# Performance work log

Hardware: AMD Instinct MI355X
Metric: run time of the kernel (lower is better)

## Reference

```python
import jax, jax.numpy as jnp
import numpy as np

B, S, D = 2, 2048, 2048
H, KVH, HD = 32, 8, 64
GROUPS = H // KVH  # 4
NEG = -1e9


def setup_inputs() -> dict:
    key = jax.random.key(0)
    ks = jax.random.split(key, 5)
    x = jax.random.normal(ks[0], (B, S, D), dtype=jnp.float32)
    # causal additive mask [1,1,S,S]
    causal = jnp.triu(jnp.full((S, S), NEG, dtype=jnp.float32), k=1)[None, None]
    Wq = jax.random.normal(ks[1], (D, D), dtype=jnp.float32) * (D ** -0.5)
    Wk = jax.random.normal(ks[2], (KVH * HD, D), dtype=jnp.float32) * (D ** -0.5)
    Wv = jax.random.normal(ks[3], (KVH * HD, D), dtype=jnp.float32) * (D ** -0.5)
    Wo = jax.random.normal(ks[4], (D, D), dtype=jnp.float32) * (D ** -0.5)
    return {"x": x, "attention_mask": causal, "Wq": Wq, "Wk": Wk, "Wv": Wv, "Wo": Wo}


def reference(x, attention_mask, Wq, Wk, Wv, Wo):
    b, s, _ = x.shape
    # projections (nn.Linear: y = x @ W.T)
    q = (x @ Wq.T).reshape(b, s, H, HD).transpose(0, 2, 1, 3)      # [b,H,s,hd]
    k = (x @ Wk.T).reshape(b, s, KVH, HD).transpose(0, 2, 1, 3)    # [b,KVH,s,hd]
    v = (x @ Wv.T).reshape(b, s, KVH, HD).transpose(0, 2, 1, 3)
    new_kv_cache = (k, v)
    # repeat_interleave over head dim for GQA
    k = jnp.repeat(k, GROUPS, axis=1)  # [b,H,s,hd]
    v = jnp.repeat(v, GROUPS, axis=1)
    scale = 1.0 / jnp.sqrt(jnp.float32(HD))
    scores = jnp.einsum('bhqd,bhkd->bhqk', q, k) * scale
    scores = scores + attention_mask
    attn = jax.nn.softmax(scores.astype(jnp.float32), axis=-1).astype(q.dtype)
    out = jnp.einsum('bhqk,bhkd->bhqd', attn, v)  # [b,H,s,hd]
    out = out.transpose(0, 2, 1, 3).reshape(b, s, H * HD)
    output = out @ Wo.T
    return (output, new_kv_cache[0], new_kv_cache[1])
```

## Files before the change

### kernel.cpp

```cpp
#include <hip/hip_runtime.h>
#include <hip/hip_bf16.h>
#include <stdint.h>

#define B_ 2
#define S_ 2048
#define D_ 2048
#define H_ 32
#define KVH_ 8
#define HD_ 64

typedef __bf16 bf16x8 __attribute__((ext_vector_type(8)));
typedef float f32x4 __attribute__((ext_vector_type(4)));

#define MFMA16(a, b, c) __builtin_amdgcn_mfma_f32_16x16x32_bf16((a), (b), (c), 0, 0, 0)

typedef __attribute__((address_space(1))) void gvoid_t;
typedef __attribute__((address_space(3))) void lvoid_t;

__device__ __forceinline__ void async_ld16(__hip_bfloat16* lds, const __hip_bfloat16* g) {
  __builtin_amdgcn_global_load_lds((gvoid_t*)(void*)(g), (lvoid_t*)(lds), 16, 0, 0);
}

__device__ __forceinline__ unsigned short f2bu(float f) {
  __hip_bfloat16 h = __float2bfloat16(f);
  return *reinterpret_cast<unsigned short*>(&h);
}

__global__ void cast_bf16_kernel(const float* __restrict__ in,
                                 unsigned short* __restrict__ out, int n4) {
  int i = blockIdx.x * blockDim.x + threadIdx.x;
  if (i >= n4) return;
  float4 v = reinterpret_cast<const float4*>(in)[i];
  ushort4 o;
  o.x = f2bu(v.x); o.y = f2bu(v.y); o.z = f2bu(v.z); o.w = f2bu(v.w);
  reinterpret_cast<ushort4*>(out)[i] = o;
}

template <int MODE, int BN, int WAVES_M, int WAVES_N>
__global__ __launch_bounds__(512, 2)
void gemm_bt2(const __hip_bfloat16* __restrict__ A,
              const __hip_bfloat16* __restrict__ W,
              float* __restrict__ Cf, __hip_bfloat16* __restrict__ Cb,
              float* __restrict__ Cf2, __hip_bfloat16* __restrict__ Cb2,
              __hip_bfloat16* __restrict__ Cb3,
              int M, int N, int K) {
  constexpr int BM = 256;
  constexpr int WM = BM / WAVES_M;
  constexpr int WN = BN / WAVES_N;
  constexpr int MR = WM / 16;
  constexpr int NR = WN / 16;
  constexpr int A_PLANE = BM * 32;
  constexpr int B_PLANE = BN * 32;
  constexpr int BUF_E = 2 * (A_PLANE + B_PLANE);
  constexpr int ACH = A_PLANE / (512 * 8);
  constexpr int BCH = B_PLANE / (512 * 8);
  constexpr int LPT = 2 * (ACH + BCH);

  __shared__ __align__(16) __hip_bfloat16 sAB[2 * BUF_E];

  const int tid = threadIdx.x;
  const int lane = tid & 63;
  const int wv = tid >> 6;
  const int l15 = lane & 15, l4 = lane >> 4;
  const int bm = blockIdx.x * BM, bn = blockIdx.y * BN;
  const int wmo = (wv / WAVES_N) * WM;
  const int wno = (wv % WAVES_N) * WN;

  const __hip_bfloat16* gA[ACH];
  const __hip_bfloat16* gB[BCH];
#pragma unroll
  for (int i = 0; i < ACH; ++i) {
    const int ch = tid + i * 512;
    const int row = ch >> 2, pc = ch & 3;
    const int c = pc ^ ((row >> 1) & 3);
    gA[i] = A + (size_t)(bm + row) * K + c * 8;
  }
#pragma unroll
  for (int i = 0; i < BCH; ++i) {
    const int ch = tid + i * 512;
    const int row = ch >> 2, pc = ch & 3;
    const int c = pc ^ ((row >> 1) & 3);
    gB[i] = W + (size_t)(bn + row) * K + c * 8;
  }

  int offA[MR], offB[NR];
#pragma unroll
  for (int mi = 0; mi < MR; ++mi) {
    const int row = wmo + mi * 16 + l15;
    offA[mi] = row * 32 + ((l4 ^ ((row >> 1) & 3)) * 8);
  }
#pragma unroll
  for (int nj = 0; nj < NR; ++nj) {
    const int row = wno + nj * 16 + l15;
    offB[nj] = row * 32 + ((l4 ^ ((row >> 1) & 3)) * 8);
  }

  f32x4 acc[MR][NR];
#pragma unroll
  for (int i = 0; i < MR; ++i)
#pragma unroll
    for (int j = 0; j < NR; ++j) acc[i][j] = f32x4{0.f, 0.f, 0.f, 0.f};

  auto stagekk = [&](int buf, int kk, int kbase) {
    __hip_bfloat16* dA = &sAB[buf * BUF_E + kk * A_PLANE];
    __hip_bfloat16* dB = &sAB[buf * BUF_E + 2 * A_PLANE + kk * B_PLANE];
#pragma unroll
    for (int i = 0; i < ACH; ++i)
      async_ld16(dA + (tid + i * 512) * 8, gA[i] + kbase);
#pragma unroll
    for (int i = 0; i < BCH; ++i)
      async_ld16(dB + (tid + i * 512) * 8, gB[i] + kbase);
  };

  const int NT = K >> 6;
  stagekk(0, 0, 0);  stagekk(0, 1, 32);
  stagekk(1, 0, 64); stagekk(1, 1, 96);
  if constexpr (LPT == 8) asm volatile("s_waitcnt vmcnt(8)" ::: "memory");
  else                    asm volatile("s_waitcnt vmcnt(6)" ::: "memory");
  __builtin_amdgcn_s_barrier();

  int cur = 0;
  for (int t = 0; t < NT; ++t) {
    const int tpre = (t + 2 < NT) ? (t + 2) : (NT - 1);
#pragma unroll
    for (int kk = 0; kk < 2; ++kk) {
      const __hip_bfloat16* pa = &sAB[cur * BUF_E + kk * A_PLANE];
      const __hip_bfloat16* pb = &sAB[cur * BUF_E + 2 * A_PLANE + kk * B_PLANE];
      bf16x8 af[MR], bfv[NR];
#pragma unroll
      for (int mi = 0; mi < MR; ++mi)
        af[mi] = *reinterpret_cast<const bf16x8*>(&pa[offA[mi]]);
#pragma unroll
      for (int nj = 0; nj < NR; ++nj)
        bfv[nj] = *reinterpret_cast<const bf16x8*>(&pb[offB[nj]]);
      __builtin_amdgcn_s_setprio(1);
#pragma unroll
      for (int mi = 0; mi < MR; ++mi)
#pragma unroll
        for (int nj = 0; nj < NR; ++nj)
          acc[mi][nj] = MFMA16(af[mi], bfv[nj], acc[mi][nj]);
      __builtin_amdgcn_s_setprio(0);
      asm volatile("s_waitcnt lgkmcnt(0)" ::: "memory");
      __builtin_amdgcn_sched_barrier(0);
      __builtin_amdgcn_s_barrier();
      stagekk(cur, kk, tpre * 64 + kk * 32);
    }
    if constexpr (LPT == 8) asm volatile("s_waitcnt vmcnt(8)" ::: "memory");
    else                    asm volatile("s_waitcnt vmcnt(6)" ::: "memory");
    __builtin_amdgcn_s_barrier();
    cur ^= 1;
  }

#pragma unroll
  for (int mi = 0; mi < MR; ++mi) {
#pragma unroll
    for (int nj = 0; nj < NR; ++nj) {
      const int col = bn + wno + nj * 16 + l15;
#pragma unroll
      for (int r = 0; r < 4; ++r) {
        const int row = bm + wmo + mi * 16 + l4 * 4 + r;
        const float v = acc[mi][nj][r];
        if (MODE == 1) {
          Cf[(size_t)row * N + col] = v;
        } else {
          if (bn < 2048) {
            Cb[(size_t)row * 2048 + col] = __float2bfloat16(v);
          } else {
            const int bb = row >> 11, s = row & 2047;
            const int kv = col - 2048;
            if (kv < 512) {
              const int g = kv >> 6, hd = kv & 63;
              const size_t idx = ((size_t)(bb * KVH_ + g) * S_ + s) * HD_ + hd;
              Cf[idx] = v;
              Cb2[idx] = __float2bfloat16(v);
            } else {
              const int vv = kv - 512;
              const int g = vv >> 6, hd = vv & 63;
              const size_t idx = ((size_t)(bb * KVH_ + g) * S_ + s) * HD_ + hd;
              Cf2[idx] = v;
              Cb3[((size_t)(bb * KVH_ + g) * HD_ + hd) * S_ + s] = __float2bfloat16(v);
            }
          }
        }
      }
    }
  }
}

__global__ __launch_bounds__(512, 4)
void attn_fused(const __hip_bfloat16* __restrict__ Qb,
                const __hip_bfloat16* __restrict__ Kb,
                const __hip_bfloat16* __restrict__ Vtb,
                __hip_bfloat16* __restrict__ AOb) {
  __shared__ __align__(16) __hip_bfloat16 sK[2][64 * 64];
  __shared__ __align__(16) __hip_bfloat16 sV[2][64 * 64];
  __shared__ __align__(16) __hip_bfloat16 sP[8 * 32 * 64];

  const int tid = threadIdx.x;
  const int lane = tid & 63;
  const int wv = tid >> 6;
  const int l15 = lane & 15, l4 = lane >> 4;
  const int qa = blockIdx.x;
  const int qb = 15 - qa;
  const int isB = wv >> 2;
  const int wq = wv & 3;
  const int qt = isB ? qb : qa;
  const int h = blockIdx.y;
  const int b = blockIdx.z;
  const int g = h >> 2;

  bf16x8 qf[2][2];
  {
    const __hip_bfloat16* Qp =
        Qb + ((size_t)(b * S_ + qt * 128 + wq * 32)) * D_ + h * HD_;
#pragma unroll
    for (int i = 0; i < 2; ++i) {
#pragma unroll
      for (int c = 0; c < 2; ++c) {
        qf[i][c] = *reinterpret_cast<const bf16x8*>(
            Qp + (size_t)(i * 16 + l15) * D_ + c * 32 + l4 * 8);
      }
    }
  }

  f32x4 oacc[2][4];
  f32x4 lacc[2];
#pragma unroll
  for (int i = 0; i < 2; ++i) {
    lacc[i] = f32x4{0.f, 0.f, 0.f, 0.f};
#pragma unroll
    for (int j = 0; j < 4; ++j) oacc[i][j] = f32x4{0.f, 0.f, 0.f, 0.f};
  }

  bf16x8 vone;
#pragma unroll
  for (int j = 0; j < 8; ++j) vone[j] = (__bf16)1.0f;

  const __hip_bfloat16* Kp = Kb + (size_t)(b * KVH_ + g) * S_ * HD_;
  const __hip_bfloat16* Vp = Vtb + (size_t)(b * KVH_ + g) * HD_ * S_;
  __hip_bfloat16* sPw = sP + wv * (32 * 64);
  const float CE = 0.125f * 1.4426950408889634f;
  const float MSUB = 8.0f;

  const int r0 = tid >> 3, c0 = (tid & 7) ^ (r0 & 7);
  const __hip_bfloat16* gk = Kp + (size_t)r0 * HD_ + c0 * 8;
  const __hip_bfloat16* gv = Vp + (size_t)r0 * S_ + c0 * 8;

  auto stage = [&](int buf) {
    async_ld16(&sK[buf][tid * 8], gk);
    async_ld16(&sV[buf][tid * 8], gv);
    gk += 64 * HD_;
    gv += 64;
  };

  auto pack = [&](f32x4 (&sc)[2][4], int koff) {
    if (koff >= 0) {
#pragma unroll
      for (int i = 0; i < 2; ++i) {
#pragma unroll
        for (int jn = 0; jn < 4; ++jn) {
          const int kp = koff + jn * 16 + l15;
#pragma unroll
          for (int r = 0; r < 4; ++r) {
            const int qp = wq * 32 + i * 16 + l4 * 4 + r;
            if (kp > qp) sc[i][jn][r] = -3.0e38f;
          }
        }
      }
    }
#pragma unroll
    for (int i = 0; i < 2; ++i) {
#pragma unroll
      for (int jj = 0; jj < 4; ++jj) {
#pragma unroll
        for (int r = 0; r < 4; ++r) {
          const float p = exp2f(fmaf(sc[i][jj][r], CE, -MSUB));
          sPw[(i * 16 + l4 * 4 + r) * 64 + ((jj ^ l4) * 16 + l15)] =
              __float2bfloat16(p);
        }
      }
    }
  };

  const int nsteps = 2 * qb + 2;
  const int kmax = isB ? nsteps : (2 * qa + 2);
  stage(0);
  for (int ki = 0; ki < nsteps; ++ki) {
    const int cur = ki & 1;
    __syncthreads();
    if (ki + 1 < nsteps) stage(cur ^ 1);
    if (ki < kmax) {
      const int ko = ((ki >> 1) == qt) ? (ki & 1) * 64 : -1;

      f32x4 sc[2][4];
#pragma unroll
      for (int jn = 0; jn < 4; ++jn) {
        const int row = jn * 16 + l15;
        const bf16x8 k0 = *reinterpret_cast<const bf16x8*>(
            &sK[cur][(row * 8 + (l4 ^ (row & 7))) * 8]);
        const bf16x8 k1 = *reinterpret_cast<const bf16x8*>(
            &sK[cur][(row * 8 + ((4 + l4) ^ (row & 7))) * 8]);
#pragma unroll
        for (int i = 0; i < 2; ++i) {
          f32x4 t = f32x4{0.f, 0.f, 0.f, 0.f};
          t = MFMA16(qf[i][0], k0, t);
          t = MFMA16(qf[i][1], k1, t);
          sc[i][jn] = t;
        }
      }

      pack(sc, ko);

      const int gr = (l15 >> 2) & 3;
#pragma unroll
      for (int kc = 0; kc < 2; ++kc) {
        bf16x8 vf[4];
#pragma unroll
        for (int jn = 0; jn < 4; ++jn) {
          const int row = jn * 16 + l15;
          vf[jn] = *reinterpret_cast<const bf16x8*>(
              &sV[cur][(row * 8 + ((kc * 4 + l4) ^ (row & 7))) * 8]);
        }
        const int pcol = (((kc * 2 + (l4 >> 1)) ^ gr) * 16 + (l4 & 1) * 8);
#pragma unroll
        for (int i = 0; i < 2; ++i) {
          const bf16x8 pf = *reinterpret_cast<const bf16x8*>(
              &sPw[(i * 16 + l15) * 64 + pcol]);
#pragma unroll
          for (int jn = 0; jn < 4; ++jn) oacc[i][jn] = MFMA16(pf, vf[jn], oacc[i][jn]);
          lacc[i] = MFMA16(pf, vone, lacc[i]);
        }
      }
    }
  }

#pragma unroll
  for (int i = 0; i < 2; ++i) {
    float inv[4];
#pragma unroll
    for (int r = 0; r < 4; ++r) inv[r] = 1.0f / lacc[i][r];
#pragma unroll
    for (int jn = 0; jn < 4; ++jn) {
#pragma unroll
      for (int r = 0; r < 4; ++r) {
        const int qp = qt * 128 + wq * 32 + i * 16 + l4 * 4 + r;
        AOb[(size_t)(b * S_ + qp) * D_ + h * HD_ + jn * 16 + l15] =
            __float2bfloat16(oacc[i][jn][r] * inv[r]);
      }
    }
  }
}

extern "C" void kernel_launch(void* const* d_in, const int* in_sizes, int n_in,
                              void* d_out, int out_size, void* d_ws, size_t ws_size,
                              hipStream_t stream) {
  (void)in_sizes; (void)n_in; (void)out_size; (void)ws_size;
  const float* x = (const float*)d_in[0];
  const float* Wq = (const float*)d_in[2];
  const float* Wk = (const float*)d_in[3];
  const float* Wv = (const float*)d_in[4];
  const float* Wo = (const float*)d_in[5];

  float* outO = (float*)d_out;
  float* outK = outO + (size_t)B_ * S_ * D_;
  float* outV = outK + (size_t)B_ * KVH_ * S_ * HD_;

  char* p = (char*)d_ws;
  __hip_bfloat16* xb    = (__hip_bfloat16*)p; p += (size_t)B_ * S_ * D_ * 2;
  __hip_bfloat16* Wqkvb = (__hip_bfloat16*)p; p += (size_t)3072 * D_ * 2;
  __hip_bfloat16* Wob   = (__hip_bfloat16*)p; p += (size_t)D_ * D_ * 2;
  __hip_bfloat16* Qbf   = (__hip_bfloat16*)p; p += (size_t)B_ * S_ * D_ * 2;
  __hip_bfloat16* Kbf   = (__hip_bfloat16*)p; p += (size_t)B_ * KVH_ * S_ * HD_ * 2;
  __hip_bfloat16* Vtb   = (__hip_bfloat16*)p; p += (size_t)B_ * KVH_ * S_ * HD_ * 2;
  __hip_bfloat16* AOb   = (__hip_bfloat16*)p; p += (size_t)B_ * S_ * D_ * 2;

  auto cast = [&](const float* src, __hip_bfloat16* dst, size_t n) {
    const int n4 = (int)(n / 4);
    cast_bf16_kernel<<<dim3((n4 + 255) / 256), dim3(256), 0, stream>>>(
        src, (unsigned short*)dst, n4);
  };
  cast(x, xb, (size_t)B_ * S_ * D_);
  cast(Wq, Wqkvb, (size_t)D_ * D_);
  cast(Wk, Wqkvb + (size_t)2048 * D_, (size_t)KVH_ * HD_ * D_);
  cast(Wv, Wqkvb + (size_t)2560 * D_, (size_t)KVH_ * HD_ * D_);
  cast(Wo, Wob, (size_t)D_ * D_);

  gemm_bt2<4, 256, 2, 4><<<dim3(16, 12), dim3(512), 0, stream>>>(
      xb, Wqkvb, outK, Qbf, outV, Kbf, Vtb, 4096, 3072, 2048);
  attn_fused<<<dim3(8, 32, 2), dim3(512), 0, stream>>>(Qbf, Kbf, Vtb, AOb);
  gemm_bt2<1, 128, 4, 2><<<dim3(16, 16), dim3(512), 0, stream>>>(
      AOb, Wob, outO, nullptr, nullptr, nullptr, nullptr, 4096, 2048, 2048);
}
```

Before: 337.7 us.

## Fuse cast kernels and restructure GEMM pipeline into split-phase prefetch

Replaces the five separate fp32-to-bf16 cast launches with one grid-stride kernel covering all tensors, removing launch overhead and tail effects. The GEMM main loop moves from a two-tile-ahead prefetch into the same buffer to a one-tile-ahead double buffer. Each k-slice is split into two halves of M, and the A and B loads for the next tile are issued between the halves so global-to-LDS traffic overlaps the MFMA work. The prefetch distance is shorter and there are more barriers per iteration, so latency hiding may suffer.

```diff
diff --git a/kernel.cpp b/kernel.cpp
--- a/kernel.cpp
+++ b/kernel.cpp
@@ -26,14 +26,35 @@
   return *reinterpret_cast<unsigned short*>(&h);
 }
 
-__global__ void cast_bf16_kernel(const float* __restrict__ in,
-                                 unsigned short* __restrict__ out, int n4) {
-  int i = blockIdx.x * blockDim.x + threadIdx.x;
-  if (i >= n4) return;
-  float4 v = reinterpret_cast<const float4*>(in)[i];
-  ushort4 o;
-  o.x = f2bu(v.x); o.y = f2bu(v.y); o.z = f2bu(v.z); o.w = f2bu(v.w);
-  reinterpret_cast<ushort4*>(out)[i] = o;
+__global__ void cast_all_kernel(const float* __restrict__ x,
+                                const float* __restrict__ wq,
+                                const float* __restrict__ wk,
+                                const float* __restrict__ wv,
+                                const float* __restrict__ wo,
+                                unsigned short* __restrict__ xb,
+                                unsigned short* __restrict__ wqkvb,
+                                unsigned short* __restrict__ wob) {
+  constexpr int NX = B_ * S_ * D_ / 4;
+  constexpr int NQ = D_ * D_ / 4;
+  constexpr int NK = KVH_ * HD_ * D_ / 4;
+  constexpr int E0 = NX;
+  constexpr int E1 = E0 + NQ;
+  constexpr int E2 = E1 + NK;
+  constexpr int E3 = E2 + NK;
+  constexpr int E4 = E3 + NQ;
+  const int stride = gridDim.x * blockDim.x;
+  for (int i = blockIdx.x * blockDim.x + threadIdx.x; i < E4; i += stride) {
+    const float* src; unsigned short* dst; int j;
+    if (i < E0)      { src = x;  dst = xb;                              j = i; }
+    else if (i < E1) { src = wq; dst = wqkvb;                           j = i - E0; }
+    else if (i < E2) { src = wk; dst = wqkvb + (size_t)2048 * D_;       j = i - E1; }
+    else if (i < E3) { src = wv; dst = wqkvb + (size_t)2560 * D_;       j = i - E2; }
+    else             { src = wo; dst = wob;                             j = i - E3; }
+    float4 v = reinterpret_cast<const float4*>(src)[j];
+    ushort4 o;
+    o.x = f2bu(v.x); o.y = f2bu(v.y); o.z = f2bu(v.z); o.w = f2bu(v.w);
+    reinterpret_cast<ushort4*>(dst)[j] = o;
+  }
 }
 
 template <int MODE, int BN, int WAVES_M, int WAVES_N>
@@ -49,12 +70,13 @@
   constexpr int WN = BN / WAVES_N;
   constexpr int MR = WM / 16;
   constexpr int NR = WN / 16;
+  constexpr int MHALF = MR / 2;
   constexpr int A_PLANE = BM * 32;
   constexpr int B_PLANE = BN * 32;
   constexpr int BUF_E = 2 * (A_PLANE + B_PLANE);
   constexpr int ACH = A_PLANE / (512 * 8);
   constexpr int BCH = B_PLANE / (512 * 8);
-  constexpr int LPT = 2 * (ACH + BCH);
+  constexpr int LPP = ACH + BCH;
 
   __shared__ __align__(16) __hip_bfloat16 sAB[2 * BUF_E];
 
@@ -101,55 +123,74 @@
 #pragma unroll
     for (int j = 0; j < NR; ++j) acc[i][j] = f32x4{0.f, 0.f, 0.f, 0.f};
 
-  auto stagekk = [&](int buf, int kk, int kbase) {
-    __hip_bfloat16* dA = &sAB[buf * BUF_E + kk * A_PLANE];
-    __hip_bfloat16* dB = &sAB[buf * BUF_E + 2 * A_PLANE + kk * B_PLANE];
-#pragma unroll
-    for (int i = 0; i < ACH; ++i)
-      async_ld16(dA + (tid + i * 512) * 8, gA[i] + kbase);
-#pragma unroll
-    for (int i = 0; i < BCH; ++i)
-      async_ld16(dB + (tid + i * 512) * 8, gB[i] + kbase);
+  auto stage_part = [&](int dstb, int kk, int tnext, int part) {
+    const int koff = tnext * 64 + kk * 32;
+    if (part == 0) {
+      __hip_bfloat16* dA = &sAB[dstb * BUF_E + kk * A_PLANE];
+#pragma unroll
+      for (int i = 0; i < ACH; ++i)
+        async_ld16(dA + (tid + i * 512) * 8, gA[i] + koff);
+    } else {
+      __hip_bfloat16* dB = &sAB[dstb * BUF_E + 2 * A_PLANE + kk * B_PLANE];
+#pragma unroll
+      for (int i = 0; i < BCH; ++i)
+        async_ld16(dB + (tid + i * 512) * 8, gB[i] + koff);
+    }
   };
 
   const int NT = K >> 6;
-  stagekk(0, 0, 0);  stagekk(0, 1, 32);
-  stagekk(1, 0, 64); stagekk(1, 1, 96);
-  if constexpr (LPT == 8) asm volatile("s_waitcnt vmcnt(8)" ::: "memory");
-  else                    asm volatile("s_waitcnt vmcnt(6)" ::: "memory");
+  stage_part(0, 0, 0, 0); stage_part(0, 0, 0, 1);
+  stage_part(0, 1, 0, 0); stage_part(0, 1, 0, 1);
+  if constexpr (LPP == 4) asm volatile("s_waitcnt vmcnt(4)" ::: "memory");
+  else                    asm volatile("s_waitcnt vmcnt(3)" ::: "memory");
   __builtin_amdgcn_s_barrier();
 
   int cur = 0;
   for (int t = 0; t < NT; ++t) {
-    const int tpre = (t + 2 < NT) ? (t + 2) : (NT - 1);
+    const int tn = (t + 1 < NT) ? (t + 1) : (NT - 1);
+    const int dstb = cur ^ 1;
 #pragma unroll
     for (int kk = 0; kk < 2; ++kk) {
       const __hip_bfloat16* pa = &sAB[cur * BUF_E + kk * A_PLANE];
       const __hip_bfloat16* pb = &sAB[cur * BUF_E + 2 * A_PLANE + kk * B_PLANE];
-      bf16x8 af[MR], bfv[NR];
-#pragma unroll
-      for (int mi = 0; mi < MR; ++mi)
+      bf16x8 bfv[NR], af[MHALF];
+#pragma unroll
+      for (int mi = 0; mi < MHALF; ++mi)
         af[mi] = *reinterpret_cast<const bf16x8*>(&pa[offA[mi]]);
 #pragma unroll
       for (int nj = 0; nj < NR; ++nj)
         bfv[nj] = *reinterpret_cast<const bf16x8*>(&pb[offB[nj]]);
+      stage_part(dstb, kk, tn, 0);
+      __builtin_amdgcn_s_barrier();
+      asm volatile("s_waitcnt lgkmcnt(0)" ::: "memory");
       __builtin_amdgcn_s_setprio(1);
 #pragma unroll
-      for (int mi = 0; mi < MR; ++mi)
+      for (int mi = 0; mi < MHALF; ++mi)
 #pragma unroll
         for (int nj = 0; nj < NR; ++nj)
           acc[mi][nj] = MFMA16(af[mi], bfv[nj], acc[mi][nj]);
       __builtin_amdgcn_s_setprio(0);
+      __builtin_amdgcn_s_barrier();
+#pragma unroll
+      for (int mi = 0; mi < MHALF; ++mi)
+        af[mi] = *reinterpret_cast<const bf16x8*>(&pa[offA[MHALF + mi]]);
+      stage_part(dstb, kk, tn, 1);
+      __builtin_amdgcn_s_barrier();
       asm volatile("s_waitcnt lgkmcnt(0)" ::: "memory");
-      __builtin_amdgcn_sched_barrier(0);
+      __builtin_amdgcn_s_setprio(1);
+#pragma unroll
+      for (int mi = 0; mi < MHALF; ++mi)
+#pragma unroll
+        for (int nj = 0; nj < NR; ++nj)
+          acc[MHALF + mi][nj] = MFMA16(af[mi], bfv[nj], acc[MHALF + mi][nj]);
+      __builtin_amdgcn_s_setprio(0);
+      if constexpr (LPP == 4) asm volatile("s_waitcnt vmcnt(4)" ::: "memory");
+      else                    asm volatile("s_waitcnt vmcnt(3)" ::: "memory");
       __builtin_amdgcn_s_barrier();
-      stagekk(cur, kk, tpre * 64 + kk * 32);
-    }
-    if constexpr (LPT == 8) asm volatile("s_waitcnt vmcnt(8)" ::: "memory");
-    else                    asm volatile("s_waitcnt vmcnt(6)" ::: "memory");
-    __builtin_amdgcn_s_barrier();
+    }
     cur ^= 1;
   }
+  asm volatile("s_waitcnt vmcnt(0)" ::: "memory");
 
 #pragma unroll
   for (int mi = 0; mi < MR; ++mi) {
@@ -374,16 +415,9 @@
   __hip_bfloat16* Vtb   = (__hip_bfloat16*)p; p += (size_t)B_ * KVH_ * S_ * HD_ * 2;
   __hip_bfloat16* AOb   = (__hip_bfloat16*)p; p += (size_t)B_ * S_ * D_ * 2;
 
-  auto cast = [&](const float* src, __hip_bfloat16* dst, size_t n) {
-    const int n4 = (int)(n / 4);
-    cast_bf16_kernel<<<dim3((n4 + 255) / 256), dim3(256), 0, stream>>>(
-        src, (unsigned short*)dst, n4);
-  };
-  cast(x, xb, (size_t)B_ * S_ * D_);
-  cast(Wq, Wqkvb, (size_t)D_ * D_);
-  cast(Wk, Wqkvb + (size_t)2048 * D_, (size_t)KVH_ * HD_ * D_);
-  cast(Wv, Wqkvb + (size_t)2560 * D_, (size_t)KVH_ * HD_ * D_);
-  cast(Wo, Wob, (size_t)D_ * D_);
+  cast_all_kernel<<<dim3(4096), dim3(256), 0, stream>>>(
+      x, Wq, Wk, Wv, Wo,
+      (unsigned short*)xb, (unsigned short*)Wqkvb, (unsigned short*)Wob);
 
   gemm_bt2<4, 256, 2, 4><<<dim3(16, 12), dim3(512), 0, stream>>>(
       xb, Wqkvb, outK, Qbf, outV, Kbf, Vtb, 4096, 3072, 2048);
```

Result: faster. 323.5 us (-4.2%).
